# Kernel optimization log

Hardware: AMD Instinct MI355X
Metric: run time of the kernel (lower is better)

## Reference

```python
import jax, jax.numpy as jnp
import numpy as np

D_MODEL = 1024
NUM_HEADS = 16
D_K = D_MODEL // NUM_HEADS  # 64
THETA = 10000.0


def apply_rope(t, positions):
    # t: [b, h, s, d], positions: [s] int
    d = t.shape[-1]
    inv_freq = 1.0 / (THETA ** (jnp.arange(0, d, 2, dtype=jnp.float32) / d))  # [d/2]
    ang = positions.astype(jnp.float32)[:, None] * inv_freq[None, :]  # [s, d/2]
    cos = jnp.cos(ang)[None, None]  # [1,1,s,d/2]
    sin = jnp.sin(ang)[None, None]
    x1 = t[..., 0::2]
    x2 = t[..., 1::2]
    r1 = x1 * cos - x2 * sin
    r2 = x1 * sin + x2 * cos
    # interleave back: [..., d/2, 2] -> [..., d]
    return jnp.stack([r1, r2], axis=-1).reshape(t.shape)


def setup_inputs() -> dict:
    key = jax.random.key(0)
    ks = jax.random.split(key, 5)
    b, s = 4, 2048
    scale = 1.0 / np.sqrt(D_MODEL)
    return {
        "x": jax.random.normal(ks[0], (b, s, D_MODEL), dtype=jnp.float32),
        "Wq": jax.random.normal(ks[1], (D_MODEL, D_MODEL), dtype=jnp.float32) * scale,
        "Wk": jax.random.normal(ks[2], (D_MODEL, D_MODEL), dtype=jnp.float32) * scale,
        "Wv": jax.random.normal(ks[3], (D_MODEL, D_MODEL), dtype=jnp.float32) * scale,
        "Wo": jax.random.normal(ks[4], (D_MODEL, D_MODEL), dtype=jnp.float32) * scale,
        "token_positions": jnp.arange(s, dtype=jnp.int32),
    }


def reference(x, Wq, Wk, Wv, Wo, token_positions):
    b, s, _ = x.shape
    # nn.Linear with no bias: y = x @ W.T
    def proj(W):
        y = jnp.einsum('bsd,ed->bse', x, W)
        return y.reshape(b, s, NUM_HEADS, D_K).transpose(0, 2, 1, 3)  # [b,h,s,dk]
    Q = apply_rope(proj(Wq), token_positions)
    K = apply_rope(proj(Wk), token_positions)
    V = proj(Wv)
    scores = jnp.einsum('bhqd,bhkd->bhqk', Q, K) / np.sqrt(D_K).astype(np.float32)
    causal = jnp.arange(s)[:, None] >= jnp.arange(s)[None, :]  # [s,s] lower-tri True
    scores = jnp.where(causal[None, None], scores, -jnp.inf)
    probs = jax.nn.softmax(scores, axis=-1)
    out = jnp.einsum('bhqk,bhkd->bhqd', probs, V)  # [b,h,s,dk]
    out = out.transpose(0, 2, 1, 3).reshape(b, s, D_MODEL)
    return jnp.einsum('bsd,ed->bse', out, Wo)
```

## Files before the change

### kernel.cpp

```cpp
#include <hip/hip_runtime.h>
#include <stdint.h>

#define SLEN 2048
#define DMODEL 1024
#define NHEADS 16
#define MTOT 8192

typedef short s16x8 __attribute__((ext_vector_type(8)));
typedef short s16x4 __attribute__((ext_vector_type(4)));
typedef float f32x4 __attribute__((ext_vector_type(4)));
typedef float f32x16 __attribute__((ext_vector_type(16)));
typedef unsigned u32x2 __attribute__((ext_vector_type(2)));
typedef unsigned u32x4 __attribute__((ext_vector_type(4)));

static __device__ __forceinline__ unsigned short f2bf(float f) {
  unsigned u = __builtin_bit_cast(unsigned, f);
  u += 0x7fffu + ((u >> 16) & 1u);
  return (unsigned short)(u >> 16);
}

static __device__ __forceinline__ unsigned cvt_pk_bf16(float lo, float hi) {
  unsigned r;
  asm("v_cvt_pk_bf16_f32 %0, %1, %2" : "=v"(r) : "v"(lo), "v"(hi));
  return r;
}

static __device__ __forceinline__ void gload_lds16(const void* g, void* l) {
  __builtin_amdgcn_global_load_lds((__attribute__((address_space(1))) void*)g,
                                   (__attribute__((address_space(3))) void*)l,
                                   16, 0, 0);
}

#define MFMA16(a, b, c) __builtin_amdgcn_mfma_f32_16x16x32_bf16(a, b, c, 0, 0, 0)
#define MFMA32(a, b, c) __builtin_amdgcn_mfma_f32_32x32x16_bf16(a, b, c, 0, 0, 0)
#define SWZ(r) ((((r) & 7) ^ (((r) >> 3) & 7)))

__global__ void __launch_bounds__(256) rope_table(const int* __restrict__ pos,
                                                  float* __restrict__ ctab,
                                                  float* __restrict__ stab) {
  int g = blockIdx.x * 256 + threadIdx.x;
  int s = g >> 5, i = g & 31;
  float p = (float)pos[s];
  float ang = p * exp2f(-(float)i * 0.41524101186092029f);
  ctab[g] = cosf(ang);
  stab[g] = sinf(ang);
}

__global__ void __launch_bounds__(256) cvt_f32_bf16(const float* __restrict__ src,
                                                    unsigned short* __restrict__ dst,
                                                    int n8) {
  int i = blockIdx.x * 256 + threadIdx.x;
  if (i >= n8) return;
  f32x4 a = ((const f32x4*)src)[i * 2];
  f32x4 b = ((const f32x4*)src)[i * 2 + 1];
  s16x8 o;
#pragma unroll
  for (int j = 0; j < 4; ++j) o[j] = (short)f2bf(a[j]);
#pragma unroll
  for (int j = 0; j < 4; ++j) o[4 + j] = (short)f2bf(b[j]);
  ((s16x8*)dst)[i] = o;
}

__global__ void __launch_bounds__(256) cvt_weights(const float* __restrict__ w0,
                                                   const float* __restrict__ w1,
                                                   const float* __restrict__ w2,
                                                   const float* __restrict__ w3,
                                                   unsigned short* __restrict__ d0,
                                                   unsigned short* __restrict__ d1,
                                                   unsigned short* __restrict__ d2,
                                                   unsigned short* __restrict__ d3) {
  int which = blockIdx.y;
  const float* src = which == 0 ? w0 : which == 1 ? w1 : which == 2 ? w2 : w3;
  unsigned short* dst = which == 0 ? d0 : which == 1 ? d1 : which == 2 ? d2 : d3;
  int i = blockIdx.x * 256 + threadIdx.x;
  f32x4 a = ((const f32x4*)src)[i * 2];
  f32x4 b = ((const f32x4*)src)[i * 2 + 1];
  s16x8 o;
#pragma unroll
  for (int j = 0; j < 4; ++j) o[j] = (short)f2bf(a[j]);
#pragma unroll
  for (int j = 0; j < 4; ++j) o[4 + j] = (short)f2bf(b[j]);
  ((s16x8*)dst)[i] = o;
}

template<int MODE>
__global__ void __launch_bounds__(256) gemm_nt(const unsigned short* __restrict__ A,
                                               const unsigned short* __restrict__ B,
                                               void* __restrict__ dstQ,
                                               void* __restrict__ dstK,
                                               void* __restrict__ dstV,
                                               const float* __restrict__ ctab,
                                               const float* __restrict__ stab,
                                               float scale) {
  __shared__ unsigned short ldsA[3][128 * 32];
  __shared__ unsigned short ldsB[3][128 * 32];
  const int tid = threadIdx.x;
  const int lane = tid & 63;
  const int wave = tid >> 6;
  const int wm = wave >> 1, wn = wave & 1;

  int m0, n0;
  if constexpr (MODE == 3) {
    int flat = blockIdx.y * 24 + blockIdx.x;
    int xcd = flat & 7, idx = flat >> 3;
    int g = idx >> 6;
    int local = idx & 63;
    int lm = local >> 3, ln = local & 7;
    m0 = (xcd * 8 + lm) * 128;
    n0 = (g * 8 + ln) * 128;
  } else {
    int flat = blockIdx.y * 8 + blockIdx.x;
    int logical = (flat & 7) * 64 + (flat >> 3);
    m0 = (logical >> 3) * 128;
    n0 = (logical & 7) * 128;
  }
  const int l15 = lane & 15, lhi = lane >> 4;

  f32x4 acc[4][4] = {};

  auto stage = [&](int buf, int kt) {
    const int kbase = kt * 32;
#pragma unroll
    for (int issue = 0; issue < 2; ++issue) {
      int c = issue * 256 + wave * 64 + lane;
      int row = c >> 2, kc = c & 3;
      int kcg = kc ^ ((row >> 1) & 3);
      gload_lds16(A + (size_t)(m0 + row) * 1024 + kbase + kcg * 8,
                  &ldsA[buf][(issue * 256 + wave * 64) * 8]);
      gload_lds16(B + (size_t)(n0 + row) * 1024 + kbase + kcg * 8,
                  &ldsB[buf][(issue * 256 + wave * 64) * 8]);
    }
  };

  stage(0, 0);
  stage(1, 1);
  for (int kt = 0; kt < 32; ++kt) {
    if (kt + 1 < 32) {
      asm volatile("s_waitcnt vmcnt(4)" ::: "memory");
    } else {
      asm volatile("s_waitcnt vmcnt(0)" ::: "memory");
    }
    __builtin_amdgcn_s_barrier();
    __builtin_amdgcn_sched_barrier(0);
    if (kt + 2 < 32) stage((kt + 2) % 3, kt + 2);

    const int buf = kt % 3;
    s16x8 af[4], bf[4];
#pragma unroll
    for (int mi = 0; mi < 4; ++mi) {
      int row = wm * 64 + mi * 16 + l15;
      int kc = lhi ^ ((row >> 1) & 3);
      af[mi] = *(const s16x8*)&ldsA[buf][row * 32 + kc * 8];
    }
#pragma unroll
    for (int ni = 0; ni < 4; ++ni) {
      int row = wn * 64 + ni * 16 + l15;
      int kc = lhi ^ ((row >> 1) & 3);
      bf[ni] = *(const s16x8*)&ldsB[buf][row * 32 + kc * 8];
    }
#pragma unroll
    for (int mi = 0; mi < 4; ++mi)
#pragma unroll
      for (int ni = 0; ni < 4; ++ni)
        acc[mi][ni] = MFMA16(af[mi], bf[ni], acc[mi][ni]);
  }

  if constexpr (MODE == 0) {
    float* dst = (float*)dstQ;
#pragma unroll
    for (int mi = 0; mi < 4; ++mi)
#pragma unroll
      for (int ni = 0; ni < 4; ++ni)
#pragma unroll
        for (int i = 0; i < 4; ++i) {
          int r = m0 + wm * 64 + mi * 16 + lhi * 4 + i;
          int n = n0 + wn * 64 + ni * 16 + l15;
          dst[(size_t)r * 1024 + n] = acc[mi][ni][i];
        }
  } else {
    const int which = n0 >> 10;
    if (which < 2) {
      unsigned short* dst = (unsigned short*)(which == 0 ? dstQ : dstK);
      const float sc = (which == 0) ? scale : 1.0f;
#pragma unroll
      for (int mi = 0; mi < 4; ++mi)
#pragma unroll
        for (int ni = 0; ni < 4; ++ni)
#pragma unroll
          for (int i = 0; i < 4; ++i) {
            int r = m0 + wm * 64 + mi * 16 + lhi * 4 + i;
            int nn = (n0 & 1023) + wn * 64 + ni * 16 + l15;
            float v = acc[mi][ni][i];
            float p = __shfl_xor(v, 1);
            int s = r & (SLEN - 1);
            int d = nn & 63;
            int fi = d >> 1;
            float c = ctab[s * 32 + fi], sn = stab[s * 32 + fi];
            float o = (d & 1) ? (p * sn + v * c) : (v * c - p * sn);
            o *= sc;
            int b = r >> 11, h = nn >> 6;
            dst[((size_t)(b * NHEADS + h) * SLEN + s) * 64 + d] = f2bf(o);
          }
    } else {
      unsigned short* dst = (unsigned short*)dstV;
#pragma unroll
      for (int mi = 0; mi < 4; ++mi)
#pragma unroll
        for (int ni = 0; ni < 4; ++ni) {
          int r0 = m0 + wm * 64 + mi * 16 + lhi * 4;
          int nn = (n0 & 1023) + wn * 64 + ni * 16 + l15;
          int b = r0 >> 11, s0 = r0 & (SLEN - 1);
          int h = nn >> 6, d = nn & 63;
          s16x4 pk;
#pragma unroll
          for (int i = 0; i < 4; ++i) pk[i] = (short)f2bf(acc[mi][ni][i]);
          *(s16x4*)&dst[((size_t)(b * NHEADS + h) * 64 + d) * SLEN + s0] = pk;
        }
    }
  }
}

__global__ void __launch_bounds__(256, 4) flash_attn(const unsigned short* __restrict__ Q,
                                                     const unsigned short* __restrict__ K,
                                                     const unsigned short* __restrict__ Vt,
                                                     unsigned short* __restrict__ Obf) {
  __shared__ unsigned short Kbuf[2][64 * 64];
  __shared__ unsigned short Vbuf[2][64 * 64];

  const int tid = threadIdx.x, lane = tid & 63, w = tid >> 6;
  const int l31 = lane & 31, h = lane >> 5;

  int id = blockIdx.x;
  int xcd = id & 7, idx = id >> 3;
  const int s_ = idx & 3;
  const int bhl = (idx >> 2) & 7;
  const int g_ = idx >> 5;
  const int mul2g = (g_ == 0) ? 0 : (g_ == 1) ? 2 : (g_ == 2) ? 3 : 1;
  const int t = 4 * (s_ ^ g_) + (s_ ^ mul2g);
  const int bh = xcd * 8 + bhl;
  const int b = bh >> 4, hd = bh & 15;

  const unsigned short* Qb = Q + (size_t)bh * SLEN * 64;
  const unsigned short* Kb = K + (size_t)bh * SLEN * 64;
  const unsigned short* Vb = Vt + (size_t)bh * 64 * SLEN;

  const int qbase = t * 128;
  const int nt = 2 * t + 2;
  const int q_abs = qbase + w * 32 + l31;
  const int qminw = qbase + w * 32;

  auto stageKV = [&](int buf, int k0) {
#pragma unroll
    for (int i = 0; i < 2; ++i) {
      int c = i * 256 + tid;
      int row = c >> 3, cg = c & 7;
      int col = ((cg ^ SWZ(row)) * 8);
      gload_lds16(Kb + (size_t)(k0 + row) * 64 + col, &Kbuf[buf][c * 8]);
      gload_lds16(Vb + (size_t)row * SLEN + k0 + col, &Vbuf[buf][c * 8]);
    }
  };

  s16x8 qf[4];
#pragma unroll
  for (int dc = 0; dc < 4; ++dc)
    qf[dc] = *(const s16x8*)&Qb[(size_t)q_abs * 64 + dc * 16 + h * 8];

  f32x16 accT[2] = {};
  float m_run = -3.0e38f, l_run = 0.f;

  stageKV(0, 0);
  for (int kt = 0; kt < nt; ++kt) {
    const int cur = kt & 1;
    const int k0 = kt * 64;
    if (kt + 1 < nt) {
      stageKV(cur ^ 1, (kt + 1) * 64);
      asm volatile("s_waitcnt vmcnt(4)" ::: "memory");
    } else {
      asm volatile("s_waitcnt vmcnt(0)" ::: "memory");
    }
    __builtin_amdgcn_s_barrier();
    __builtin_amdgcn_sched_barrier(0);

    {
      f32x16 sacc[2] = {};
#pragma unroll
      for (int kb = 0; kb < 2; ++kb) {
#pragma unroll
        for (int dc = 0; dc < 4; ++dc) {
          int r = kb * 32 + l31;
          int g = dc * 2 + h;
          s16x8 kf = *(const s16x8*)&Kbuf[cur][r * 64 + ((g ^ SWZ(r)) * 8)];
          sacc[kb] = MFMA32(kf, qf[dc], sacc[kb]);
        }
      }

      if (k0 + 63 > qminw) {
#pragma unroll
        for (int kb = 0; kb < 2; ++kb)
#pragma unroll
          for (int r = 0; r < 16; ++r) {
            int k_abs = k0 + kb * 32 + (r & 3) + 8 * (r >> 2) + 4 * h;
            if (k_abs > q_abs) sacc[kb][r] = -3.0e38f;
          }
      }

      float mx = sacc[0][0];
#pragma unroll
      for (int kb = 0; kb < 2; ++kb)
#pragma unroll
        for (int r = 0; r < 16; ++r) mx = fmaxf(mx, sacc[kb][r]);
      mx = fmaxf(mx, __shfl_xor(mx, 32));

      if (!__all(mx <= m_run)) {
        float mnew = fmaxf(m_run, mx);
        float facv = exp2f(m_run - mnew);
        m_run = mnew;
        l_run *= facv;
#pragma unroll
        for (int db = 0; db < 2; ++db)
#pragma unroll
          for (int r = 0; r < 16; ++r) accT[db][r] *= facv;
      }

      float sum = 0.f;
#pragma unroll
      for (int kb = 0; kb < 2; ++kb)
#pragma unroll
        for (int r = 0; r < 16; ++r) {
          float p = exp2f(sacc[kb][r] - m_run);
          sacc[kb][r] = p;
          sum += p;
        }
      l_run += sum + __shfl_xor(sum, 32);

      unsigned Hv[8][2];
#pragma unroll
      for (int kb = 0; kb < 2; ++kb)
#pragma unroll
        for (int q4 = 0; q4 < 4; ++q4) {
          Hv[kb * 4 + q4][0] = cvt_pk_bf16(sacc[kb][q4 * 4 + 0], sacc[kb][q4 * 4 + 1]);
          Hv[kb * 4 + q4][1] = cvt_pk_bf16(sacc[kb][q4 * 4 + 2], sacc[kb][q4 * 4 + 3]);
        }
      s16x8 pf[4];
#pragma unroll
      for (int c = 0; c < 4; ++c) {
        unsigned loc0 = h ? Hv[2 * c + 1][0] : Hv[2 * c][0];
        unsigned loc1 = h ? Hv[2 * c + 1][1] : Hv[2 * c][1];
        unsigned snd0 = h ? Hv[2 * c][0] : Hv[2 * c + 1][0];
        unsigned snd1 = h ? Hv[2 * c][1] : Hv[2 * c + 1][1];
        unsigned rcv0 = (unsigned)__shfl_xor((int)snd0, 32);
        unsigned rcv1 = (unsigned)__shfl_xor((int)snd1, 32);
        u32x4 tv;
        tv[0] = h ? rcv0 : loc0;
        tv[1] = h ? rcv1 : loc1;
        tv[2] = h ? loc0 : rcv0;
        tv[3] = h ? loc1 : rcv1;
        pf[c] = __builtin_bit_cast(s16x8, tv);
      }

#pragma unroll
      for (int db = 0; db < 2; ++db)
#pragma unroll
        for (int kc = 0; kc < 4; ++kc) {
          int r = db * 32 + l31;
          int g = kc * 2 + h;
          s16x8 vf = *(const s16x8*)&Vbuf[cur][r * 64 + ((g ^ SWZ(r)) * 8)];
          accT[db] = MFMA32(vf, pf[kc], accT[db]);
        }
    }

    __builtin_amdgcn_sched_barrier(0);
    __builtin_amdgcn_s_barrier();
  }

  float linv = 1.f / l_run;
#pragma unroll
  for (int db = 0; db < 2; ++db)
#pragma unroll
    for (int q4 = 0; q4 < 4; ++q4) {
      u32x2 pk;
      pk[0] = cvt_pk_bf16(accT[db][q4 * 4 + 0] * linv, accT[db][q4 * 4 + 1] * linv);
      pk[1] = cvt_pk_bf16(accT[db][q4 * 4 + 2] * linv, accT[db][q4 * 4 + 3] * linv);
      int d0 = db * 32 + 8 * q4 + 4 * h;
      *(u32x2*)&Obf[((size_t)(b * SLEN + q_abs)) * DMODEL + hd * 64 + d0] = pk;
    }
}

extern "C" void kernel_launch(void* const* d_in, const int* in_sizes, int n_in,
                              void* d_out, int out_size, void* d_ws, size_t ws_size,
                              hipStream_t stream) {
  const float* x  = (const float*)d_in[0];
  const float* Wq = (const float*)d_in[1];
  const float* Wk = (const float*)d_in[2];
  const float* Wv = (const float*)d_in[3];
  const float* Wo = (const float*)d_in[4];
  const int* pos  = (const int*)d_in[5];
  float* out = (float*)d_out;

  char* ws = (char*)d_ws;
  size_t off = 0;
  auto take = [&](size_t bytes) {
    char* p = ws + off;
    off += (bytes + 255) & ~(size_t)255;
    return p;
  };
  unsigned short* xbf  = (unsigned short*)take((size_t)MTOT * DMODEL * 2);
  unsigned short* wqkv = (unsigned short*)take((size_t)3 * DMODEL * DMODEL * 2);
  unsigned short* wobf = (unsigned short*)take((size_t)DMODEL * DMODEL * 2);
  unsigned short* Qs   = (unsigned short*)take((size_t)64 * SLEN * 64 * 2);
  unsigned short* Ks   = (unsigned short*)take((size_t)64 * SLEN * 64 * 2);
  unsigned short* Vt   = (unsigned short*)take((size_t)64 * 64 * SLEN * 2);
  unsigned short* Obf  = (unsigned short*)take((size_t)MTOT * DMODEL * 2);
  float* ctab = (float*)take((size_t)SLEN * 32 * 4);
  float* stab = (float*)take((size_t)SLEN * 32 * 4);

  rope_table<<<256, 256, 0, stream>>>(pos, ctab, stab);
  cvt_f32_bf16<<<4096, 256, 0, stream>>>(x, xbf, MTOT * DMODEL / 8);
  cvt_weights<<<dim3(512, 4), 256, 0, stream>>>(
      Wq, Wk, Wv, Wo,
      wqkv, wqkv + (size_t)DMODEL * DMODEL, wqkv + (size_t)2 * DMODEL * DMODEL, wobf);

  gemm_nt<3><<<dim3(24, 64), 256, 0, stream>>>(xbf, wqkv, Qs, Ks, Vt,
                                               ctab, stab, 0.18033688011112042f);

  flash_attn<<<1024, 256, 0, stream>>>(Qs, Ks, Vt, Obf);

  gemm_nt<0><<<dim3(8, 64), 256, 0, stream>>>(Obf, wobf, out, nullptr, nullptr,
                                              nullptr, nullptr, 1.0f);
}
```

Measured before the change: 190.8 us.

## Remove P cross-lane shuffles by permuting V fragment reads; raise MFMA priority

In the attention inner loop, the PV MFMA no longer does cross-half shuffles to rearrange the P fragment. Instead it reads V from shared memory in a permuted k order (two 8-byte loads per fragment) so the P registers can be used exactly as the QK MFMA produced them. It also wraps the MFMA blocks in s_setprio and splits the max and sum reductions into four independent chains for more ILP. The cost is twice as many narrower LDS reads for V, and the permuted k ordering must be correct.

```diff
diff --git a/kernel.cpp b/kernel.cpp
--- a/kernel.cpp
+++ b/kernel.cpp
@@ -283,6 +283,7 @@
 
     {
       f32x16 sacc[2] = {};
+      __builtin_amdgcn_s_setprio(1);
 #pragma unroll
       for (int kb = 0; kb < 2; ++kb) {
 #pragma unroll
@@ -293,6 +294,7 @@
           sacc[kb] = MFMA32(kf, qf[dc], sacc[kb]);
         }
       }
+      __builtin_amdgcn_s_setprio(0);
 
       if (k0 + 63 > qminw) {
 #pragma unroll
@@ -304,11 +306,18 @@
           }
       }
 
-      float mx = sacc[0][0];
-#pragma unroll
-      for (int kb = 0; kb < 2; ++kb)
-#pragma unroll
-        for (int r = 0; r < 16; ++r) mx = fmaxf(mx, sacc[kb][r]);
+      float p0 = fmaxf(sacc[0][0], sacc[1][0]);
+      float p1 = fmaxf(sacc[0][1], sacc[1][1]);
+      float p2 = fmaxf(sacc[0][2], sacc[1][2]);
+      float p3 = fmaxf(sacc[0][3], sacc[1][3]);
+#pragma unroll
+      for (int r = 4; r < 16; r += 4) {
+        p0 = fmaxf(p0, fmaxf(sacc[0][r + 0], sacc[1][r + 0]));
+        p1 = fmaxf(p1, fmaxf(sacc[0][r + 1], sacc[1][r + 1]));
+        p2 = fmaxf(p2, fmaxf(sacc[0][r + 2], sacc[1][r + 2]));
+        p3 = fmaxf(p3, fmaxf(sacc[0][r + 3], sacc[1][r + 3]));
+      }
+      float mx = fmaxf(fmaxf(p0, p1), fmaxf(p2, p3));
       mx = fmaxf(mx, __shfl_xor(mx, 32));
 
       if (!__all(mx <= m_run)) {
@@ -322,16 +331,22 @@
           for (int r = 0; r < 16; ++r) accT[db][r] *= facv;
       }
 
-      float sum = 0.f;
+      float s0 = 0.f, s1 = 0.f, s2 = 0.f, s3 = 0.f;
 #pragma unroll
       for (int kb = 0; kb < 2; ++kb)
 #pragma unroll
-        for (int r = 0; r < 16; ++r) {
-          float p = exp2f(sacc[kb][r] - m_run);
-          sacc[kb][r] = p;
-          sum += p;
-        }
-      l_run += sum + __shfl_xor(sum, 32);
+        for (int r = 0; r < 16; r += 4) {
+          float e0 = exp2f(sacc[kb][r + 0] - m_run);
+          float e1 = exp2f(sacc[kb][r + 1] - m_run);
+          float e2 = exp2f(sacc[kb][r + 2] - m_run);
+          float e3 = exp2f(sacc[kb][r + 3] - m_run);
+          sacc[kb][r + 0] = e0; sacc[kb][r + 1] = e1;
+          sacc[kb][r + 2] = e2; sacc[kb][r + 3] = e3;
+          s0 += e0; s1 += e1; s2 += e2; s3 += e3;
+        }
+      float sum = (s0 + s1) + (s2 + s3);
+      sum += __shfl_xor(sum, 32);
+      l_run += sum;
 
       unsigned Hv[8][2];
 #pragma unroll
@@ -341,32 +356,26 @@
           Hv[kb * 4 + q4][0] = cvt_pk_bf16(sacc[kb][q4 * 4 + 0], sacc[kb][q4 * 4 + 1]);
           Hv[kb * 4 + q4][1] = cvt_pk_bf16(sacc[kb][q4 * 4 + 2], sacc[kb][q4 * 4 + 3]);
         }
-      s16x8 pf[4];
-#pragma unroll
-      for (int c = 0; c < 4; ++c) {
-        unsigned loc0 = h ? Hv[2 * c + 1][0] : Hv[2 * c][0];
-        unsigned loc1 = h ? Hv[2 * c + 1][1] : Hv[2 * c][1];
-        unsigned snd0 = h ? Hv[2 * c][0] : Hv[2 * c + 1][0];
-        unsigned snd1 = h ? Hv[2 * c][1] : Hv[2 * c + 1][1];
-        unsigned rcv0 = (unsigned)__shfl_xor((int)snd0, 32);
-        unsigned rcv1 = (unsigned)__shfl_xor((int)snd1, 32);
-        u32x4 tv;
-        tv[0] = h ? rcv0 : loc0;
-        tv[1] = h ? rcv1 : loc1;
-        tv[2] = h ? loc0 : rcv0;
-        tv[3] = h ? loc1 : rcv1;
-        pf[c] = __builtin_bit_cast(s16x8, tv);
+
+      __builtin_amdgcn_s_setprio(1);
+#pragma unroll
+      for (int db = 0; db < 2; ++db) {
+        int r = db * 32 + l31;
+        const char* rowp = (const char*)&Vbuf[cur][r * 64];
+#pragma unroll
+        for (int kc = 0; kc < 4; ++kc) {
+          u32x2 vlo = *(const u32x2*)(rowp + (((2 * kc) ^ SWZ(r)) * 16) + 8 * h);
+          u32x2 vhi = *(const u32x2*)(rowp + (((2 * kc + 1) ^ SWZ(r)) * 16) + 8 * h);
+          u32x4 vv;
+          vv[0] = vlo[0]; vv[1] = vlo[1]; vv[2] = vhi[0]; vv[3] = vhi[1];
+          u32x4 pv;
+          pv[0] = Hv[2 * kc][0]; pv[1] = Hv[2 * kc][1];
+          pv[2] = Hv[2 * kc + 1][0]; pv[3] = Hv[2 * kc + 1][1];
+          accT[db] = MFMA32(__builtin_bit_cast(s16x8, vv),
+                            __builtin_bit_cast(s16x8, pv), accT[db]);
+        }
       }
-
-#pragma unroll
-      for (int db = 0; db < 2; ++db)
-#pragma unroll
-        for (int kc = 0; kc < 4; ++kc) {
-          int r = db * 32 + l31;
-          int g = kc * 2 + h;
-          s16x8 vf = *(const s16x8*)&Vbuf[cur][r * 64 + ((g ^ SWZ(r)) * 8)];
-          accT[db] = MFMA32(vf, pf[kc], accT[db]);
-        }
+      __builtin_amdgcn_s_setprio(0);
     }
 
     __builtin_amdgcn_sched_barrier(0);
```

After: 191.9 us. About the same (+0.6%).
